# Kernel optimization log

Measured on AMD Instinct MI355X. Metric: run time of the kernel, lower is better.

The kernel has to match this reference:

```python
import jax, jax.numpy as jnp
import numpy as np

N_QUBITS = 4
N_LAYERS = 2


def _ry(theta):
    # PennyLane RY(theta) = [[cos(t/2), -sin(t/2)], [sin(t/2), cos(t/2)]]
    c = jnp.cos(theta / 2)
    s = jnp.sin(theta / 2)
    return jnp.stack([jnp.stack([c, -s]), jnp.stack([s, c])]).astype(jnp.complex64)


def _rz(theta):
    # PennyLane RZ(theta) = diag(exp(-i t/2), exp(+i t/2))
    e = jnp.exp(-0.5j * theta.astype(jnp.complex64))
    return jnp.diag(jnp.stack([e, jnp.conj(e)]))


def _apply_1q(state, U, wire):
    # state: (2,)*N_QUBITS complex; contract U into axis `wire`
    state = jnp.tensordot(U, state, axes=((1,), (wire,)))
    return jnp.moveaxis(state, 0, wire)


def _cnot(state, ctrl, tgt):
    s = jnp.moveaxis(state, ctrl, 0)
    t2 = tgt - 1 if tgt > ctrl else tgt
    s1 = jnp.flip(s[1], axis=t2)  # X on target where control == 1
    return jnp.moveaxis(jnp.stack([s[0], s1]), 0, ctrl)


def _circuit(angles, weights):
    # angles: (N_QUBITS,), weights: (N_LAYERS, N_QUBITS, 2)
    state = jnp.zeros((2,) * N_QUBITS, jnp.complex64).at[(0,) * N_QUBITS].set(1.0)
    for i in range(N_QUBITS):
        state = _apply_1q(state, _ry(angles[i]), i)
    for l in range(N_LAYERS):
        for i in range(N_QUBITS):
            state = _apply_1q(state, _ry(weights[l, i, 0]), i)
            state = _apply_1q(state, _rz(weights[l, i, 1]), i)
        for i in range(N_QUBITS - 1):
            state = _cnot(state, i, i + 1)
        state = _cnot(state, N_QUBITS - 1, 0)
    probs = jnp.abs(state) ** 2
    p = probs.reshape(2, -1).sum(axis=1)  # marginal on wire 0
    return p[0] - p[1]  # <Z_0>


def setup_inputs() -> dict:
    key = jax.random.key(0)
    ks = jax.random.split(key, 6)
    B = 65536
    return {
        "x": jax.random.normal(ks[0], (B, 256), jnp.float32),
        "W1": jax.random.normal(ks[1], (64, 256), jnp.float32) * 0.0625,
        "b1": jax.random.normal(ks[2], (64,), jnp.float32) * 0.01,
        "W2": jax.random.normal(ks[3], (4, 64), jnp.float32) * 0.125,
        "b2": jax.random.normal(ks[4], (4,), jnp.float32) * 0.01,
        "q_weights": jax.random.normal(ks[5], (N_LAYERS, N_QUBITS, 2), jnp.float32) * 0.1,
    }


def reference(x, W1, b1, W2, b2, q_weights):
    h = jax.nn.relu(x @ W1.T + b1)          # [B, 64]
    angles = jnp.tanh(h @ W2.T + b2)         # [B, 4]
    z = jax.vmap(lambda a: _circuit(a, q_weights))(angles)  # [B]
    return z[:, None]                        # [B, 1]
```

## Files before the change

kernel.cpp:

```cpp
#include <hip/hip_runtime.h>
#include <math.h>

typedef _Float16 half8   __attribute__((ext_vector_type(8)));
typedef _Float16 half4v  __attribute__((ext_vector_type(4)));
typedef float    float4v __attribute__((ext_vector_type(4)));

#define BM    64
#define KDIM  256
#define WSTR  264
#define HSW   65

__global__ __launch_bounds__(256, 4)
void qc_fused(const float* __restrict__ x,
              const float* __restrict__ W1,
              const float* __restrict__ b1,
              const float* __restrict__ W2,
              const float* __restrict__ b2,
              const float* __restrict__ qw,
              float* __restrict__ out)
{
    __shared__ __align__(16) unsigned char smem_raw[BM * WSTR * 2];
    __shared__ float w2s[256];
    __shared__ float b1s[64];
    __shared__ float b2s[4];
    __shared__ float trig[32];
    __shared__ float angs[BM * 4];

    _Float16* wh = (_Float16*)smem_raw;
    float*    hs = (float*)smem_raw;

    const int tid  = threadIdx.x;
    const int lane = tid & 63;
    const int wv   = tid >> 6;
    const int m    = lane & 15;
    const int q    = lane >> 4;
    const int row0 = blockIdx.x * BM;

    const float* xrow = x + (size_t)(row0 + wv * 16 + m) * KDIM + q * 8;
    float4v xv[16];
    #pragma unroll
    for (int f = 0; f < 8; ++f) {
        xv[2 * f]     = *(const float4v*)(xrow + f * 32);
        xv[2 * f + 1] = *(const float4v*)(xrow + f * 32 + 4);
    }

    w2s[tid] = W2[tid];
    if (tid < 64) b1s[tid] = b1[tid];
    if (tid < 4)  b2s[tid] = b2[tid];
    if (tid < 8) {
        int l = tid >> 2, i = tid & 3;
        float wy = qw[(l * 4 + i) * 2 + 0];
        float wz = qw[(l * 4 + i) * 2 + 1];
        float sy, cy, sz, cz;
        sincosf(0.5f * wy, &sy, &cy);
        sincosf(0.5f * wz, &sz, &cz);
        trig[(l * 4 + i) * 4 + 0] = cy;
        trig[(l * 4 + i) * 4 + 1] = sy;
        trig[(l * 4 + i) * 4 + 2] = cz;
        trig[(l * 4 + i) * 4 + 3] = sz;
    }

    {
        const int rw = tid >> 2;
        const int c0 = (tid & 3) * 4;
        const float* wrow = W1 + (size_t)rw * KDIM;
        #pragma unroll
        for (int j = 0; j < 16; ++j) {
            float4v v = *(const float4v*)(wrow + c0 + 16 * j);
            half4v h;
            h[0] = (_Float16)v[0]; h[1] = (_Float16)v[1];
            h[2] = (_Float16)v[2]; h[3] = (_Float16)v[3];
            *(half4v*)&wh[rw * WSTR + c0 + 16 * j] = h;
        }
    }

    half8 afr[8];
    #pragma unroll
    for (int f = 0; f < 8; ++f) {
        afr[f][0] = (_Float16)xv[2 * f][0];
        afr[f][1] = (_Float16)xv[2 * f][1];
        afr[f][2] = (_Float16)xv[2 * f][2];
        afr[f][3] = (_Float16)xv[2 * f][3];
        afr[f][4] = (_Float16)xv[2 * f + 1][0];
        afr[f][5] = (_Float16)xv[2 * f + 1][1];
        afr[f][6] = (_Float16)xv[2 * f + 1][2];
        afr[f][7] = (_Float16)xv[2 * f + 1][3];
    }

    __syncthreads();

    float4v acc[4] = {};
    #pragma unroll
    for (int f = 0; f < 8; ++f) {
        const int ko = f * 32 + q * 8;
        #pragma unroll
        for (int b = 0; b < 4; ++b) {
            half8 bf = *(const half8*)&wh[(16 * b + m) * WSTR + ko];
            acc[b] = __builtin_amdgcn_mfma_f32_16x16x32_f16(afr[f], bf, acc[b], 0, 0, 0);
        }
    }
    __syncthreads();

    #pragma unroll
    for (int b = 0; b < 4; ++b) {
        #pragma unroll
        for (int i = 0; i < 4; ++i) {
            int row = wv * 16 + q * 4 + i;
            int col = 16 * b + m;
            hs[row * HSW + col] = fmaxf(acc[b][i] + b1s[col], 0.0f);
        }
    }
    __syncthreads();

    {
        int r = tid & 63, qi = tid >> 6;
        float s = b2s[qi];
        #pragma unroll 8
        for (int k = 0; k < 64; ++k)
            s = fmaf(hs[r * HSW + k], w2s[qi * 64 + k], s);
        angs[r * 4 + qi] = tanhf(s);
    }
    __syncthreads();

    if (tid < 64) {
        float ca[4], sa[4];
        #pragma unroll
        for (int i = 0; i < 4; ++i)
            __sincosf(0.5f * angs[tid * 4 + i], &sa[i], &ca[i]);

        float re[16], im[16];
        #pragma unroll
        for (int idx = 0; idx < 16; ++idx) {
            re[idx] = (idx & 8 ? sa[0] : ca[0]) * (idx & 4 ? sa[1] : ca[1]) *
                      (idx & 2 ? sa[2] : ca[2]) * (idx & 1 ? sa[3] : ca[3]);
            im[idx] = 0.0f;
        }
        #pragma unroll
        for (int l = 0; l < 2; ++l) {
            #pragma unroll
            for (int i = 0; i < 4; ++i) {
                const float cy = trig[(l * 4 + i) * 4 + 0];
                const float sy = trig[(l * 4 + i) * 4 + 1];
                const float cz = trig[(l * 4 + i) * 4 + 2];
                const float sz = trig[(l * 4 + i) * 4 + 3];
                const int mq = 8 >> i;
                #pragma unroll
                for (int idx = 0; idx < 16; ++idx) {
                    if (!(idx & mq)) {
                        int j = idx | mq;
                        float ar = re[idx], ai = im[idx], br = re[j], bi = im[j];
                        re[idx] = fmaf(cy, ar, -sy * br);
                        im[idx] = fmaf(cy, ai, -sy * bi);
                        re[j]   = fmaf(sy, ar,  cy * br);
                        im[j]   = fmaf(sy, ai,  cy * bi);
                    }
                }
                #pragma unroll
                for (int idx = 0; idx < 16; ++idx) {
                    float sgn = (idx & mq) ? sz : -sz;
                    float ar = re[idx], ai = im[idx];
                    re[idx] = fmaf(ar, cz, -ai * sgn);
                    im[idx] = fmaf(ar, sgn, ai * cz);
                }
            }
            #pragma unroll
            for (int c = 0; c < 4; ++c) {
                int t  = (c + 1) & 3;
                int mc = 8 >> c, mt = 8 >> t;
                #pragma unroll
                for (int idx = 0; idx < 16; ++idx) {
                    if ((idx & mc) && !(idx & mt)) {
                        int j = idx | mt;
                        float tr = re[idx]; re[idx] = re[j]; re[j] = tr;
                        float ti = im[idx]; im[idx] = im[j]; im[j] = ti;
                    }
                }
            }
        }
        float z = 0.0f;
        #pragma unroll
        for (int idx = 0; idx < 16; ++idx) {
            float p = re[idx] * re[idx] + im[idx] * im[idx];
            z += (idx & 8) ? -p : p;
        }
        out[row0 + tid] = z;
    }
}

extern "C" void kernel_launch(void* const* d_in, const int* in_sizes, int n_in,
                              void* d_out, int out_size, void* d_ws, size_t ws_size,
                              hipStream_t stream) {
    const float* x  = (const float*)d_in[0];
    const float* W1 = (const float*)d_in[1];
    const float* b1 = (const float*)d_in[2];
    const float* W2 = (const float*)d_in[3];
    const float* b2 = (const float*)d_in[4];
    const float* qw = (const float*)d_in[5];
    float* out = (float*)d_out;
    const int B = in_sizes[0] / KDIM;
    qc_fused<<<B / BM, 256, 0, stream>>>(x, W1, b1, W2, b2, qw, out);
}
```

Measured before the change: 107.6 us.

## Pre-convert W1 to fp16 in a separate kernel and read it from global memory

Measured after the change: 117.9 us. +9.6%, slower.

```diff
diff --git a/kernel.cpp b/kernel.cpp
--- a/kernel.cpp
+++ b/kernel.cpp
@@ -7,27 +7,30 @@
 
 #define BM    64
 #define KDIM  256
-#define WSTR  264
 #define HSW   65
+
+__global__ void w1_cvt(const float* __restrict__ W1, _Float16* __restrict__ w1h)
+{
+    int i = (blockIdx.x * 256 + threadIdx.x) * 4;
+    float4v v = *(const float4v*)(W1 + i);
+    half4v h;
+    h[0] = (_Float16)v[0]; h[1] = (_Float16)v[1];
+    h[2] = (_Float16)v[2]; h[3] = (_Float16)v[3];
+    *(half4v*)(w1h + i) = h;
+}
 
 __global__ __launch_bounds__(256, 4)
 void qc_fused(const float* __restrict__ x,
-              const float* __restrict__ W1,
+              const _Float16* __restrict__ w1h,
               const float* __restrict__ b1,
               const float* __restrict__ W2,
               const float* __restrict__ b2,
               const float* __restrict__ qw,
               float* __restrict__ out)
 {
-    __shared__ __align__(16) unsigned char smem_raw[BM * WSTR * 2];
-    __shared__ float w2s[256];
-    __shared__ float b1s[64];
-    __shared__ float b2s[4];
+    __shared__ float hs[BM * HSW];
+    __shared__ float angs[BM * 4];
     __shared__ float trig[32];
-    __shared__ float angs[BM * 4];
-
-    _Float16* wh = (_Float16*)smem_raw;
-    float*    hs = (float*)smem_raw;
 
     const int tid  = threadIdx.x;
     const int lane = tid & 63;
@@ -36,17 +39,6 @@
     const int q    = lane >> 4;
     const int row0 = blockIdx.x * BM;
 
-    const float* xrow = x + (size_t)(row0 + wv * 16 + m) * KDIM + q * 8;
-    float4v xv[16];
-    #pragma unroll
-    for (int f = 0; f < 8; ++f) {
-        xv[2 * f]     = *(const float4v*)(xrow + f * 32);
-        xv[2 * f + 1] = *(const float4v*)(xrow + f * 32 + 4);
-    }
-
-    w2s[tid] = W2[tid];
-    if (tid < 64) b1s[tid] = b1[tid];
-    if (tid < 4)  b2s[tid] = b2[tid];
     if (tid < 8) {
         int l = tid >> 2, i = tid & 3;
         float wy = qw[(l * 4 + i) * 2 + 0];
@@ -60,34 +52,21 @@
         trig[(l * 4 + i) * 4 + 3] = sz;
     }
 
-    {
-        const int rw = tid >> 2;
-        const int c0 = (tid & 3) * 4;
-        const float* wrow = W1 + (size_t)rw * KDIM;
-        #pragma unroll
-        for (int j = 0; j < 16; ++j) {
-            float4v v = *(const float4v*)(wrow + c0 + 16 * j);
-            half4v h;
-            h[0] = (_Float16)v[0]; h[1] = (_Float16)v[1];
-            h[2] = (_Float16)v[2]; h[3] = (_Float16)v[3];
-            *(half4v*)&wh[rw * WSTR + c0 + 16 * j] = h;
-        }
-    }
-
+    const float* xrow = x + (size_t)(row0 + wv * 16 + m) * KDIM + q * 8;
     half8 afr[8];
     #pragma unroll
     for (int f = 0; f < 8; ++f) {
-        afr[f][0] = (_Float16)xv[2 * f][0];
-        afr[f][1] = (_Float16)xv[2 * f][1];
-        afr[f][2] = (_Float16)xv[2 * f][2];
-        afr[f][3] = (_Float16)xv[2 * f][3];
-        afr[f][4] = (_Float16)xv[2 * f + 1][0];
-        afr[f][5] = (_Float16)xv[2 * f + 1][1];
-        afr[f][6] = (_Float16)xv[2 * f + 1][2];
-        afr[f][7] = (_Float16)xv[2 * f + 1][3];
+        float4v v0 = *(const float4v*)(xrow + f * 32);
+        float4v v1 = *(const float4v*)(xrow + f * 32 + 4);
+        afr[f][0] = (_Float16)v0[0]; afr[f][1] = (_Float16)v0[1];
+        afr[f][2] = (_Float16)v0[2]; afr[f][3] = (_Float16)v0[3];
+        afr[f][4] = (_Float16)v1[0]; afr[f][5] = (_Float16)v1[1];
+        afr[f][6] = (_Float16)v1[2]; afr[f][7] = (_Float16)v1[3];
     }
 
-    __syncthreads();
+    float b1v[4];
+    #pragma unroll
+    for (int b = 0; b < 4; ++b) b1v[b] = b1[16 * b + m];
 
     float4v acc[4] = {};
     #pragma unroll
@@ -95,11 +74,10 @@
         const int ko = f * 32 + q * 8;
         #pragma unroll
         for (int b = 0; b < 4; ++b) {
-            half8 bf = *(const half8*)&wh[(16 * b + m) * WSTR + ko];
+            half8 bf = *(const half8*)(w1h + (size_t)(16 * b + m) * KDIM + ko);
             acc[b] = __builtin_amdgcn_mfma_f32_16x16x32_f16(afr[f], bf, acc[b], 0, 0, 0);
         }
     }
-    __syncthreads();
 
     #pragma unroll
     for (int b = 0; b < 4; ++b) {
@@ -107,17 +85,17 @@
         for (int i = 0; i < 4; ++i) {
             int row = wv * 16 + q * 4 + i;
             int col = 16 * b + m;
-            hs[row * HSW + col] = fmaxf(acc[b][i] + b1s[col], 0.0f);
+            hs[row * HSW + col] = fmaxf(acc[b][i] + b1v[b], 0.0f);
         }
     }
     __syncthreads();
 
     {
         int r = tid & 63, qi = tid >> 6;
-        float s = b2s[qi];
+        float s = b2[qi];
         #pragma unroll 8
         for (int k = 0; k < 64; ++k)
-            s = fmaf(hs[r * HSW + k], w2s[qi * 64 + k], s);
+            s = fmaf(hs[r * HSW + k], W2[qi * 64 + k], s);
         angs[r * 4 + qi] = tanhf(s);
     }
     __syncthreads();
@@ -197,6 +175,9 @@
     const float* b2 = (const float*)d_in[4];
     const float* qw = (const float*)d_in[5];
     float* out = (float*)d_out;
+    _Float16* w1h = (_Float16*)d_ws;
+
+    w1_cvt<<<16, 256, 0, stream>>>(W1, w1h);
     const int B = in_sizes[0] / KDIM;
-    qc_fused<<<B / BM, 256, 0, stream>>>(x, W1, b1, W2, b2, qw, out);
+    qc_fused<<<B / BM, 256, 0, stream>>>(x, w1h, b1, W2, b2, qw, out);
 }
```

## Double rows per block to reuse W1 tile and transpose hidden layout

Applied to the files above, without the earlier changes.

Result: no change. 106.9 us (-0.7%).

```diff
diff --git a/kernel.cpp b/kernel.cpp
--- a/kernel.cpp
+++ b/kernel.cpp
@@ -5,12 +5,12 @@
 typedef _Float16 half4v  __attribute__((ext_vector_type(4)));
 typedef float    float4v __attribute__((ext_vector_type(4)));
 
-#define BM    64
+#define BM    128
 #define KDIM  256
 #define WSTR  264
-#define HSW   65
-
-__global__ __launch_bounds__(256, 4)
+#define HTS   132
+
+__global__ __launch_bounds__(256, 2)
 void qc_fused(const float* __restrict__ x,
               const float* __restrict__ W1,
               const float* __restrict__ b1,
@@ -19,15 +19,12 @@
               const float* __restrict__ qw,
               float* __restrict__ out)
 {
-    __shared__ __align__(16) unsigned char smem_raw[BM * WSTR * 2];
-    __shared__ float w2s[256];
-    __shared__ float b1s[64];
-    __shared__ float b2s[4];
+    __shared__ __align__(16) unsigned char smem_raw[64 * WSTR * 2];
+    __shared__ float angs[BM * 4];
     __shared__ float trig[32];
-    __shared__ float angs[BM * 4];
-
-    _Float16* wh = (_Float16*)smem_raw;
-    float*    hs = (float*)smem_raw;
+
+    _Float16* whs = (_Float16*)smem_raw;
+    float*    hst = (float*)smem_raw;
 
     const int tid  = threadIdx.x;
     const int lane = tid & 63;
@@ -36,17 +33,6 @@
     const int q    = lane >> 4;
     const int row0 = blockIdx.x * BM;
 
-    const float* xrow = x + (size_t)(row0 + wv * 16 + m) * KDIM + q * 8;
-    float4v xv[16];
-    #pragma unroll
-    for (int f = 0; f < 8; ++f) {
-        xv[2 * f]     = *(const float4v*)(xrow + f * 32);
-        xv[2 * f + 1] = *(const float4v*)(xrow + f * 32 + 4);
-    }
-
-    w2s[tid] = W2[tid];
-    if (tid < 64) b1s[tid] = b1[tid];
-    if (tid < 4)  b2s[tid] = b2[tid];
     if (tid < 8) {
         int l = tid >> 2, i = tid & 3;
         float wy = qw[(l * 4 + i) * 2 + 0];
@@ -60,6 +46,21 @@
         trig[(l * 4 + i) * 4 + 3] = sz;
     }
 
+    const float* xr0 = x + (size_t)(row0 + wv * 32 +      m) * KDIM + q * 8;
+    const float* xr1 = x + (size_t)(row0 + wv * 32 + 16 + m) * KDIM + q * 8;
+    float4v xv0[16], xv1[16];
+    #pragma unroll
+    for (int f = 0; f < 8; ++f) {
+        xv0[2 * f]     = *(const float4v*)(xr0 + f * 32);
+        xv0[2 * f + 1] = *(const float4v*)(xr0 + f * 32 + 4);
+        xv1[2 * f]     = *(const float4v*)(xr1 + f * 32);
+        xv1[2 * f + 1] = *(const float4v*)(xr1 + f * 32 + 4);
+    }
+
+    float b1v[4];
+    #pragma unroll
+    for (int b = 0; b < 4; ++b) b1v[b] = b1[16 * b + m];
+
     {
         const int rw = tid >> 2;
         const int c0 = (tid & 3) * 4;
@@ -70,59 +71,68 @@
             half4v h;
             h[0] = (_Float16)v[0]; h[1] = (_Float16)v[1];
             h[2] = (_Float16)v[2]; h[3] = (_Float16)v[3];
-            *(half4v*)&wh[rw * WSTR + c0 + 16 * j] = h;
-        }
-    }
-
-    half8 afr[8];
+            *(half4v*)&whs[rw * WSTR + c0 + 16 * j] = h;
+        }
+    }
+
+    half8 af0[8], af1[8];
     #pragma unroll
     for (int f = 0; f < 8; ++f) {
-        afr[f][0] = (_Float16)xv[2 * f][0];
-        afr[f][1] = (_Float16)xv[2 * f][1];
-        afr[f][2] = (_Float16)xv[2 * f][2];
-        afr[f][3] = (_Float16)xv[2 * f][3];
-        afr[f][4] = (_Float16)xv[2 * f + 1][0];
-        afr[f][5] = (_Float16)xv[2 * f + 1][1];
-        afr[f][6] = (_Float16)xv[2 * f + 1][2];
-        afr[f][7] = (_Float16)xv[2 * f + 1][3];
-    }
-
-    __syncthreads();
-
-    float4v acc[4] = {};
+        #pragma unroll
+        for (int j = 0; j < 4; ++j) {
+            af0[f][j]     = (_Float16)xv0[2 * f][j];
+            af0[f][4 + j] = (_Float16)xv0[2 * f + 1][j];
+            af1[f][j]     = (_Float16)xv1[2 * f][j];
+            af1[f][4 + j] = (_Float16)xv1[2 * f + 1][j];
+        }
+    }
+
+    __syncthreads();
+
+    float4v acc[2][4] = {};
     #pragma unroll
     for (int f = 0; f < 8; ++f) {
         const int ko = f * 32 + q * 8;
         #pragma unroll
         for (int b = 0; b < 4; ++b) {
-            half8 bf = *(const half8*)&wh[(16 * b + m) * WSTR + ko];
-            acc[b] = __builtin_amdgcn_mfma_f32_16x16x32_f16(afr[f], bf, acc[b], 0, 0, 0);
-        }
-    }
-    __syncthreads();
-
-    #pragma unroll
-    for (int b = 0; b < 4; ++b) {
-        #pragma unroll
-        for (int i = 0; i < 4; ++i) {
-            int row = wv * 16 + q * 4 + i;
+            half8 bf = *(const half8*)&whs[(16 * b + m) * WSTR + ko];
+            acc[0][b] = __builtin_amdgcn_mfma_f32_16x16x32_f16(af0[f], bf, acc[0][b], 0, 0, 0);
+            acc[1][b] = __builtin_amdgcn_mfma_f32_16x16x32_f16(af1[f], bf, acc[1][b], 0, 0, 0);
+        }
+    }
+    __syncthreads();
+
+    #pragma unroll
+    for (int a = 0; a < 2; ++a) {
+        #pragma unroll
+        for (int b = 0; b < 4; ++b) {
+            int row = wv * 32 + a * 16 + q * 4;
             int col = 16 * b + m;
-            hs[row * HSW + col] = fmaxf(acc[b][i] + b1s[col], 0.0f);
+            float4v v;
+            #pragma unroll
+            for (int i = 0; i < 4; ++i) v[i] = fmaxf(acc[a][b][i] + b1v[b], 0.0f);
+            *(float4v*)&hst[col * HTS + row] = v;
         }
     }
     __syncthreads();
 
     {
-        int r = tid & 63, qi = tid >> 6;
-        float s = b2s[qi];
+        int r = tid & 127, pair = tid >> 7;
+        float s0 = b2[2 * pair], s1 = b2[2 * pair + 1];
+        const float* w2a = W2 + (2 * pair) * 64;
+        const float* w2b = W2 + (2 * pair + 1) * 64;
         #pragma unroll 8
-        for (int k = 0; k < 64; ++k)
-            s = fmaf(hs[r * HSW + k], w2s[qi * 64 + k], s);
-        angs[r * 4 + qi] = tanhf(s);
-    }
-    __syncthreads();
-
-    if (tid < 64) {
+        for (int k = 0; k < 64; ++k) {
+            float hv = hst[k * HTS + r];
+            s0 = fmaf(hv, w2a[k], s0);
+            s1 = fmaf(hv, w2b[k], s1);
+        }
+        angs[r * 4 + 2 * pair]     = tanhf(s0);
+        angs[r * 4 + 2 * pair + 1] = tanhf(s1);
+    }
+    __syncthreads();
+
+    if (tid < BM) {
         float ca[4], sa[4];
         #pragma unroll
         for (int i = 0; i < 4; ++i)
```
